# Performance work log

Measured on AMD Instinct MI355X. Metric: run time of the kernel, lower is better.

## Reference

```python
import jax, jax.numpy as jnp
import numpy as np

TAU = 0.1
BN_EPS = 1e-5


def setup_inputs() -> dict:
    key = jax.random.key(0)
    ks = jax.random.split(key, 10)
    bs, C, N, E, P = 2, 256, 4096, 2048, 32
    return {
        "vertex_feat": jax.random.normal(ks[0], (bs, C, N), dtype=jnp.float32),
        "incidence": jax.random.uniform(ks[1], (bs, N, E), dtype=jnp.float32),
        "inv_edge_degree": jax.random.uniform(ks[2], (bs, E, E), dtype=jnp.float32),
        "inv_vertex_degree": jax.random.uniform(ks[3], (bs, N, N), dtype=jnp.float32),
        "edge_scale": jax.random.uniform(ks[4], (bs, E, 1), dtype=jnp.float32),
        "proj_w": jax.random.normal(ks[5], (P, C), dtype=jnp.float32) * (1.0 / np.sqrt(C)),
        "bn_gamma": jax.random.uniform(ks[6], (P,), dtype=jnp.float32, minval=0.5, maxval=1.5),
        "bn_beta": jax.random.normal(ks[7], (P,), dtype=jnp.float32) * 0.1,
        "bn_mean": jax.random.normal(ks[8], (P,), dtype=jnp.float32) * 0.1,
        "bn_var": jax.random.uniform(ks[9], (P,), dtype=jnp.float32, minval=0.5, maxval=1.5),
    }


def reference(vertex_feat, incidence, inv_edge_degree, inv_vertex_degree, edge_scale,
              proj_w, bn_gamma, bn_beta, bn_mean, bn_var):
    # proj: 1x1 Conv1d [bs,C,N] -> [bs,P,N], then eval-mode BatchNorm1d over channel P
    K = jnp.einsum("pc,bcn->bpn", proj_w, vertex_feat)
    scale = (bn_gamma / jnp.sqrt(bn_var + BN_EPS))[None, :, None]
    K = (K - bn_mean[None, :, None]) * scale + bn_beta[None, :, None]
    K = jnp.transpose(K, (0, 2, 1))  # [bs, N, P]

    # edge prototypes: incidence^T @ K, normalized by inverse edge degree
    proto = jnp.einsum("bne,bnp->bep", incidence, K)          # [bs, E, P]
    proto = jnp.einsum("bef,bfp->bep", inv_edge_degree, proto)

    # squared L2 cost: ||proto_e||^2 + ||K_n||^2 - 2 <proto_e, K_n>
    K_sq = jnp.sum(K * K, axis=-1)[:, None, :]                 # [bs, 1, N]
    proto_sq = jnp.sum(proto * proto, axis=-1, keepdims=True)  # [bs, E, 1]
    inner = jnp.einsum("bep,bnp->ben", proto, K)               # [bs, E, N]
    cost = proto_sq + K_sq - 2.0 * inner

    weights = jax.nn.softmax(-cost / (TAU + 1e-8), axis=-1)    # [bs, E, N]

    # aggregate vertex features into edges
    edge_feat = jnp.einsum("ben,bcn->bec", weights, vertex_feat)   # [bs, E, C]
    edge_feat = jnp.einsum("bef,bfc->bec", inv_edge_degree, edge_feat)
    return jnp.transpose(edge_feat, (0, 2, 1))  # [bs, C, E]
```

## Files before the change

### kernel.cpp

```cpp
#include <hip/hip_runtime.h>
#include <math.h>

#define BS 2
#define C_DIM 256
#define N_DIM 4096
#define E_DIM 2048
#define P_DIM 32
#define NS1 32
#define FS2 8

typedef __attribute__((ext_vector_type(8))) short short8;
typedef __attribute__((ext_vector_type(4))) float f32x4;

__device__ __forceinline__ unsigned short f2bf(float f) {
  unsigned u = __float_as_uint(f);
  return (unsigned short)((u + 0x7FFFu + ((u >> 16) & 1u)) >> 16);
}

__global__ __launch_bounds__(256) void k_proj(
    const float* __restrict__ vf, const float* __restrict__ pw,
    const float* __restrict__ gamma, const float* __restrict__ beta,
    const float* __restrict__ mean, const float* __restrict__ var,
    float* __restrict__ Kf, float* __restrict__ Ksq) {
  __shared__ float w_s[P_DIM * C_DIM];
  __shared__ float part_s[4][64][P_DIM + 1];
  __shared__ float kt_s[64][P_DIM + 1];
  __shared__ float sc_s[P_DIM], sb_s[P_DIM], sm_s[P_DIM];

  const int tid = threadIdx.x;
  const int b = blockIdx.x >> 6;
  const int n0 = (blockIdx.x & 63) << 6;

  for (int i = tid; i < P_DIM * C_DIM; i += 256) w_s[i] = pw[i];
  if (tid < P_DIM) {
    sc_s[tid] = gamma[tid] / sqrtf(var[tid] + 1e-5f);
    sb_s[tid] = beta[tid];
    sm_s[tid] = mean[tid];
  }
  __syncthreads();

  const int nl = tid & 63, cs = tid >> 6;
  const float* vbase = vf + (size_t)b * C_DIM * N_DIM + n0 + nl;
  float acc[P_DIM];
#pragma unroll
  for (int p = 0; p < P_DIM; ++p) acc[p] = 0.f;
#pragma unroll 4
  for (int cc = 0; cc < 64; ++cc) {
    int c = cs * 64 + cc;
    float v = vbase[(size_t)c * N_DIM];
    const float* wc = &w_s[c];
#pragma unroll
    for (int p = 0; p < P_DIM; ++p) acc[p] = fmaf(wc[p * C_DIM], v, acc[p]);
  }
#pragma unroll
  for (int p = 0; p < P_DIM; ++p) part_s[cs][nl][p] = acc[p];
  __syncthreads();

  for (int i = tid; i < 64 * P_DIM; i += 256) {
    int n_l = i >> 5, p = i & 31;
    float s = ((part_s[0][n_l][p] + part_s[1][n_l][p]) + part_s[2][n_l][p]) +
              part_s[3][n_l][p];
    float k = (s - sm_s[p]) * sc_s[p] + sb_s[p];
    Kf[((size_t)(b * N_DIM + n0 + n_l)) * P_DIM + p] = k;
    kt_s[n_l][p] = k;
  }
  __syncthreads();
  if (tid < 64) {
    float q = 0.f;
#pragma unroll
    for (int p = 0; p < P_DIM; ++p) q = fmaf(kt_s[tid][p], kt_s[tid][p], q);
    Ksq[b * N_DIM + n0 + tid] = q;
  }
}

__global__ __launch_bounds__(256) void k_transpose(const float* __restrict__ vf,
                                                   float* __restrict__ VT) {
  __shared__ float t_s[64][65];
  const int tid = threadIdx.x;
  const int b = blockIdx.x >> 8;
  const int n0 = ((blockIdx.x >> 2) & 63) << 6;
  const int c0 = (blockIdx.x & 3) << 6;
  const float* src = vf + (size_t)b * C_DIM * N_DIM;
#pragma unroll
  for (int i = 0; i < 16; ++i) {
    int idx = tid + i * 256;
    int n_l = idx & 63, c_l = idx >> 6;
    t_s[c_l][n_l] = src[(size_t)(c0 + c_l) * N_DIM + n0 + n_l];
  }
  __syncthreads();
  float* dst = VT + (size_t)b * N_DIM * C_DIM;
#pragma unroll
  for (int i = 0; i < 16; ++i) {
    int idx = tid + i * 256;
    int c_l = idx & 63, n_l = idx >> 6;
    dst[(size_t)(n0 + n_l) * C_DIM + c0 + c_l] = t_s[c_l][n_l];
  }
}

__global__ __launch_bounds__(256) void k_proto1(const float* __restrict__ inc,
                                                const float* __restrict__ Kf,
                                                float* __restrict__ part) {
  __shared__ float k_s[64][P_DIM];
  const int tid = threadIdx.x;
  const int b = blockIdx.x >> 7;
  const int et = (blockIdx.x >> 5) & 3;
  const int ns = blockIdx.x & 31;
  const int e0 = et << 9;
  const int nbase = ns << 7;

  float acc0[P_DIM], acc1[P_DIM];
#pragma unroll
  for (int p = 0; p < P_DIM; ++p) { acc0[p] = 0.f; acc1[p] = 0.f; }

  for (int nt = 0; nt < 2; ++nt) {
    int n0 = nbase + nt * 64;
#pragma unroll
    for (int i = 0; i < 8; ++i) {
      int idx = tid + i * 256;
      ((float*)k_s)[idx] = Kf[((size_t)(b * N_DIM + n0)) * P_DIM + idx];
    }
    __syncthreads();
#pragma unroll 8
    for (int nn = 0; nn < 64; ++nn) {
      const float* irow = inc + ((size_t)(b * N_DIM + n0 + nn)) * E_DIM + e0;
      float va = irow[tid];
      float vb = irow[tid + 256];
      const float4* kv4 = (const float4*)k_s[nn];
#pragma unroll
      for (int q = 0; q < 8; ++q) {
        float4 kv = kv4[q];
        acc0[4 * q + 0] = fmaf(va, kv.x, acc0[4 * q + 0]);
        acc0[4 * q + 1] = fmaf(va, kv.y, acc0[4 * q + 1]);
        acc0[4 * q + 2] = fmaf(va, kv.z, acc0[4 * q + 2]);
        acc0[4 * q + 3] = fmaf(va, kv.w, acc0[4 * q + 3]);
        acc1[4 * q + 0] = fmaf(vb, kv.x, acc1[4 * q + 0]);
        acc1[4 * q + 1] = fmaf(vb, kv.y, acc1[4 * q + 1]);
        acc1[4 * q + 2] = fmaf(vb, kv.z, acc1[4 * q + 2]);
        acc1[4 * q + 3] = fmaf(vb, kv.w, acc1[4 * q + 3]);
      }
    }
    __syncthreads();
  }
  float* dst0 = part + (size_t)ns * (BS * E_DIM * P_DIM) +
                ((size_t)(b * E_DIM + e0 + tid)) * P_DIM;
  float* dst1 = dst0 + 256 * P_DIM;
#pragma unroll
  for (int q = 0; q < 8; ++q) {
    ((float4*)dst0)[q] = make_float4(acc0[4 * q + 0], acc0[4 * q + 1],
                                     acc0[4 * q + 2], acc0[4 * q + 3]);
    ((float4*)dst1)[q] = make_float4(acc1[4 * q + 0], acc1[4 * q + 1],
                                     acc1[4 * q + 2], acc1[4 * q + 3]);
  }
}

__global__ __launch_bounds__(256) void k_red32(const float* __restrict__ part,
                                               float* __restrict__ outp) {
  int g = blockIdx.x * 256 + threadIdx.x;
  float v = 0.f;
#pragma unroll
  for (int s = 0; s < NS1; ++s)
    v += part[(size_t)s * (BS * E_DIM * P_DIM) + g];
  outp[g] = v;
}

__global__ __launch_bounds__(256) void k_proto2(const float* __restrict__ ied,
                                                const float* __restrict__ proto1,
                                                float* __restrict__ part,
                                                short* __restrict__ ied_h) {
  __shared__ float inv_s[128][33];
  __shared__ float p1_s[32][P_DIM];
  const int tid = threadIdx.x;
  const int b = blockIdx.x >> 7;
  const int et = (blockIdx.x >> 3) & 15;
  const int fs = blockIdx.x & 7;
  const int e0 = et << 7;
  const int fbase = fs << 8;
  const int e_l = tid & 63, pg = tid >> 6;

  float acc0[8], acc1[8];
#pragma unroll
  for (int q = 0; q < 8; ++q) { acc0[q] = 0.f; acc1[q] = 0.f; }

  for (int ft = 0; ft < 8; ++ft) {
    int f0 = fbase + ft * 32;
    __syncthreads();
#pragma unroll
    for (int i = 0; i < 16; ++i) {
      int idx = tid + i * 256;
      int e_r = idx >> 5, f_l = idx & 31;
      size_t gidx = ((size_t)(b * E_DIM + e0 + e_r)) * E_DIM + f0 + f_l;
      float v = ied[gidx];
      inv_s[e_r][f_l] = v;
      ied_h[gidx] = (short)f2bf(v);
    }
#pragma unroll
    for (int i = 0; i < 4; ++i) {
      int idx = tid + i * 256;
      ((float*)p1_s)[idx] = proto1[((size_t)(b * E_DIM + f0)) * P_DIM + idx];
    }
    __syncthreads();
#pragma unroll
    for (int ff = 0; ff < 32; ++ff) {
      float a0 = inv_s[e_l][ff];
      float a1 = inv_s[e_l + 64][ff];
      const float4* pv4 = (const float4*)&p1_s[ff][pg * 8];
      float4 pv0 = pv4[0], pv1 = pv4[1];
      acc0[0] = fmaf(a0, pv0.x, acc0[0]);
      acc0[1] = fmaf(a0, pv0.y, acc0[1]);
      acc0[2] = fmaf(a0, pv0.z, acc0[2]);
      acc0[3] = fmaf(a0, pv0.w, acc0[3]);
      acc0[4] = fmaf(a0, pv1.x, acc0[4]);
      acc0[5] = fmaf(a0, pv1.y, acc0[5]);
      acc0[6] = fmaf(a0, pv1.z, acc0[6]);
      acc0[7] = fmaf(a0, pv1.w, acc0[7]);
      acc1[0] = fmaf(a1, pv0.x, acc1[0]);
      acc1[1] = fmaf(a1, pv0.y, acc1[1]);
      acc1[2] = fmaf(a1, pv0.z, acc1[2]);
      acc1[3] = fmaf(a1, pv0.w, acc1[3]);
      acc1[4] = fmaf(a1, pv1.x, acc1[4]);
      acc1[5] = fmaf(a1, pv1.y, acc1[5]);
      acc1[6] = fmaf(a1, pv1.z, acc1[6]);
      acc1[7] = fmaf(a1, pv1.w, acc1[7]);
    }
  }
  float* dst0 = part + (size_t)fs * (BS * E_DIM * P_DIM) +
                ((size_t)(b * E_DIM + e0 + e_l)) * P_DIM + pg * 8;
  float* dst1 = dst0 + 64 * P_DIM;
  ((float4*)dst0)[0] = make_float4(acc0[0], acc0[1], acc0[2], acc0[3]);
  ((float4*)dst0)[1] = make_float4(acc0[4], acc0[5], acc0[6], acc0[7]);
  ((float4*)dst1)[0] = make_float4(acc1[0], acc1[1], acc1[2], acc1[3]);
  ((float4*)dst1)[1] = make_float4(acc1[4], acc1[5], acc1[6], acc1[7]);
}

__global__ __launch_bounds__(256) void k_red8sq(const float* __restrict__ part,
                                                float* __restrict__ proto,
                                                float* __restrict__ psq) {
  int g = blockIdx.x * 256 + threadIdx.x;
  float v = 0.f;
#pragma unroll
  for (int s = 0; s < FS2; ++s)
    v += part[(size_t)s * (BS * E_DIM * P_DIM) + g];
  proto[g] = v;
  float q = v * v;
#pragma unroll
  for (int m = 1; m <= 16; m <<= 1) q += __shfl_xor(q, m, 64);
  if ((threadIdx.x & 31) == 0) psq[g >> 5] = q;
}

__global__ __launch_bounds__(256) void k_gmax(const float* __restrict__ Kf,
                                              const float* __restrict__ Ksq,
                                              const float* __restrict__ proto,
                                              float* __restrict__ chunkg) {
  __shared__ float a_s[P_DIM][64];
  __shared__ float b_s[P_DIM][64];
  __shared__ float q_s[64];
  const int tid = threadIdx.x;
  const int b = blockIdx.x >> 8;
  const int et = (blockIdx.x >> 3) & 31;
  const int ns = blockIdx.x & 7;
  const int e0 = et << 6;
  const int n0b = ns << 9;

  {
    int p = tid >> 6, e = tid & 63;
#pragma unroll
    for (int r = 0; r < 8; ++r)
      a_s[p + r * 4][e] =
          proto[((size_t)(b * E_DIM + e0 + e)) * P_DIM + p + r * 4];
  }
  const int te = tid >> 4, tn = tid & 15;
  float gm[4];
#pragma unroll
  for (int i = 0; i < 4; ++i) gm[i] = -INFINITY;

  for (int t = 0; t < 8; ++t) {
    const int n0 = n0b + t * 64;
    __syncthreads();
    {
      int p = tid >> 6, n = tid & 63;
#pragma unroll
      for (int r = 0; r < 8; ++r)
        b_s[p + r * 4][n] =
            Kf[((size_t)(b * N_DIM + n0 + n)) * P_DIM + p + r * 4];
      if (tid < 64) q_s[tid] = Ksq[b * N_DIM + n0 + tid];
    }
    __syncthreads();

    float acc[4][4];
#pragma unroll
    for (int i = 0; i < 4; ++i)
#pragma unroll
      for (int j = 0; j < 4; ++j) acc[i][j] = 0.f;

#pragma unroll
    for (int p = 0; p < P_DIM; ++p) {
      float4 av = *(const float4*)&a_s[p][te << 2];
      float4 bv = *(const float4*)&b_s[p][tn << 2];
      acc[0][0] = fmaf(av.x, bv.x, acc[0][0]);
      acc[0][1] = fmaf(av.x, bv.y, acc[0][1]);
      acc[0][2] = fmaf(av.x, bv.z, acc[0][2]);
      acc[0][3] = fmaf(av.x, bv.w, acc[0][3]);
      acc[1][0] = fmaf(av.y, bv.x, acc[1][0]);
      acc[1][1] = fmaf(av.y, bv.y, acc[1][1]);
      acc[1][2] = fmaf(av.y, bv.z, acc[1][2]);
      acc[1][3] = fmaf(av.y, bv.w, acc[1][3]);
      acc[2][0] = fmaf(av.z, bv.x, acc[2][0]);
      acc[2][1] = fmaf(av.z, bv.y, acc[2][1]);
      acc[2][2] = fmaf(av.z, bv.z, acc[2][2]);
      acc[2][3] = fmaf(av.z, bv.w, acc[2][3]);
      acc[3][0] = fmaf(av.w, bv.x, acc[3][0]);
      acc[3][1] = fmaf(av.w, bv.y, acc[3][1]);
      acc[3][2] = fmaf(av.w, bv.z, acc[3][2]);
      acc[3][3] = fmaf(av.w, bv.w, acc[3][3]);
    }
#pragma unroll
    for (int i = 0; i < 4; ++i)
#pragma unroll
      for (int j = 0; j < 4; ++j) {
        float g = fmaf(2.0f, acc[i][j], -q_s[(tn << 2) + j]);
        gm[i] = fmaxf(gm[i], g);
      }

    if (t & 1) {
#pragma unroll
      for (int i = 0; i < 4; ++i) {
        float v = gm[i];
        v = fmaxf(v, __shfl_xor(v, 1, 64));
        v = fmaxf(v, __shfl_xor(v, 2, 64));
        v = fmaxf(v, __shfl_xor(v, 4, 64));
        v = fmaxf(v, __shfl_xor(v, 8, 64));
        if (tn == 0)
          chunkg[((size_t)(b * E_DIM + e0 + (te << 2) + i)) * 32 + (ns << 2) +
                 (t >> 1)] = v;
        gm[i] = -INFINITY;
      }
    }
  }
}

__device__ __forceinline__ float edge_logit(const float* __restrict__ Kb,
                                            const float* __restrict__ Qb,
                                            const float* pr, float psqv,
                                            int n) {
  const float4* kp = (const float4*)(Kb + (size_t)n * P_DIM);
  float i0 = 0.f, i1 = 0.f, i2 = 0.f, i3 = 0.f;
#pragma unroll
  for (int q = 0; q < 8; ++q) {
    float4 kv = kp[q];
    i0 = fmaf(pr[4 * q + 0], kv.x, i0);
    i1 = fmaf(pr[4 * q + 1], kv.y, i1);
    i2 = fmaf(pr[4 * q + 2], kv.z, i2);
    i3 = fmaf(pr[4 * q + 3], kv.w, i3);
  }
  float inner = (i0 + i1) + (i2 + i3);
  float cost = fmaf(-2.0f, inner, psqv + Qb[n]);
  const float tau_eps = 0.1f + 1e-8f;
  return (-cost) / tau_eps;
}

__global__ __launch_bounds__(256) void k_sparse(
    const float* __restrict__ Kf, const float* __restrict__ Ksq,
    const float* __restrict__ proto, const float* __restrict__ psq,
    const float* __restrict__ VT, const float* __restrict__ chunkg,
    float* __restrict__ EF0) {
  const int tid = threadIdx.x;
  const int lane = tid & 63;
  const int eg = blockIdx.x * 4 + (tid >> 6);
  const int b = eg >> 11;
  const float* Kb = Kf + (size_t)b * N_DIM * P_DIM;
  const float* Qb = Ksq + (size_t)b * N_DIM;

  float cg = (lane < 32) ? chunkg[(size_t)eg * 32 + lane] : -INFINITY;
  float gmax = cg;
#pragma unroll
  for (int m = 1; m <= 32; m <<= 1) gmax = fmaxf(gmax, __shfl_xor(gmax, m, 64));
  unsigned long long live = __ballot(cg > gmax - 20.0f);

  float pr[P_DIM];
  const float* pe = proto + (size_t)eg * P_DIM;
#pragma unroll
  for (int p = 0; p < P_DIM; ++p) pr[p] = pe[p];
  const float psqv = psq[eg];

  float L = -INFINITY;
  unsigned long long m0 = live;
  while (m0) {
    int c = __ffsll(m0) - 1;
    m0 &= m0 - 1;
    int n = (c << 7) + lane;
    L = fmaxf(L, edge_logit(Kb, Qb, pr, psqv, n));
    L = fmaxf(L, edge_logit(Kb, Qb, pr, psqv, n + 64));
  }
#pragma unroll
  for (int m = 1; m <= 32; m <<= 1) L = fmaxf(L, __shfl_xor(L, m, 64));

  float4 acc = make_float4(0.f, 0.f, 0.f, 0.f);
  float sw = 0.f;
  const float* Vb = VT + (size_t)b * N_DIM * C_DIM;
  m0 = live;
  while (m0) {
    int c = __ffsll(m0) - 1;
    m0 &= m0 - 1;
#pragma unroll
    for (int h = 0; h < 2; ++h) {
      int n = (c << 7) + (h << 6) + lane;
      float l = edge_logit(Kb, Qb, pr, psqv, n);
      float d = l - L;
      float wgt = (d > -25.0f) ? expf(d) : 0.f;
      sw += wgt;
      unsigned long long hits = __ballot(wgt > 0.f);
      while (hits) {
        int src = __ffsll(hits) - 1;
        hits &= hits - 1;
        float wv = __shfl(wgt, src, 64);
        int nv = (c << 7) + (h << 6) + src;
        const float4 vrow =
            *(const float4*)(Vb + (size_t)nv * C_DIM + (lane << 2));
        acc.x = fmaf(wv, vrow.x, acc.x);
        acc.y = fmaf(wv, vrow.y, acc.y);
        acc.z = fmaf(wv, vrow.z, acc.z);
        acc.w = fmaf(wv, vrow.w, acc.w);
      }
    }
  }
#pragma unroll
  for (int m = 1; m <= 32; m <<= 1) sw += __shfl_xor(sw, m, 64);

  float* dst = EF0 + (size_t)eg * C_DIM + (lane << 2);
  *(float4*)dst =
      make_float4(acc.x / sw, acc.y / sw, acc.z / sw, acc.w / sw);
}

__global__ __launch_bounds__(256) void k_ef0t(const float* __restrict__ EF0,
                                              short* __restrict__ EF0t) {
  __shared__ short sh[64][72];
  const int tid = threadIdx.x;
  const int b = blockIdx.x >> 7;
  const int ft = (blockIdx.x >> 2) & 31;
  const int ct = blockIdx.x & 3;
  const int f0 = ft << 6, c0 = ct << 6;
#pragma unroll
  for (int i = 0; i < 4; ++i) {
    int idx = tid + i * 256;
    int f_l = idx >> 4, cc = idx & 15;
    float4 v =
        *(const float4*)&EF0[((size_t)(b * E_DIM + f0 + f_l)) * C_DIM + c0 +
                             cc * 4];
    sh[cc * 4 + 0][f_l] = (short)f2bf(v.x);
    sh[cc * 4 + 1][f_l] = (short)f2bf(v.y);
    sh[cc * 4 + 2][f_l] = (short)f2bf(v.z);
    sh[cc * 4 + 3][f_l] = (short)f2bf(v.w);
  }
  __syncthreads();
#pragma unroll
  for (int i = 0; i < 2; ++i) {
    int idx = tid + i * 256;
    int c_l = idx >> 3, ch = idx & 7;
    short8 v = *(const short8*)&sh[c_l][ch * 8];
    *(short8*)&EF0t[((size_t)(b * C_DIM + c0 + c_l)) * E_DIM + f0 + ch * 8] = v;
  }
}

__device__ __forceinline__ short8 lds_frag(const short* s, int row, int k) {
  int off = (((row << 6) + k) << 1) ^ ((row & 7) << 4);
  return *(const short8*)((const char*)s + off);
}
__device__ __forceinline__ void lds_put(short* s, int row, int k, short8 v) {
  int off = (((row << 6) + k) << 1) ^ ((row & 7) << 4);
  *(short8*)((char*)s + off) = v;
}

__global__ __launch_bounds__(256) void k_final_mfma(
    const short* __restrict__ Ah, const short* __restrict__ Bh,
    float* __restrict__ out) {
  __shared__ short As[2][64 * 64];
  __shared__ short Bs[2][64 * 64];
  __shared__ float Cs[64][68];

  const int tid = threadIdx.x;
  const int lane = tid & 63;
  const int w = tid >> 6;
  const int ct = blockIdx.x & 3;
  const int et = (blockIdx.x >> 2) & 31;
  const int b = blockIdx.x >> 7;
  const int e0 = et << 6, c0 = ct << 6;

  const int we = (w >> 1) << 5;
  const int wc = (w & 1) << 5;
  const int row = tid >> 2, ch = tid & 3;

  const short* gA = Ah + ((size_t)(b * E_DIM + e0 + row)) * E_DIM;
  const short* gB = Bh + ((size_t)(b * C_DIM + c0 + row)) * E_DIM;

  f32x4 z = {0.f, 0.f, 0.f, 0.f};
  f32x4 acc00 = z, acc01 = z, acc10 = z, acc11 = z;

  {
    const short8* pa = (const short8*)(gA + ch * 16);
    const short8* pb = (const short8*)(gB + ch * 16);
    short8 a0 = pa[0], a1 = pa[1];
    short8 b0 = pb[0], b1 = pb[1];
    lds_put(As[0], row, ch * 16, a0);
    lds_put(As[0], row, ch * 16 + 8, a1);
    lds_put(Bs[0], row, ch * 16, b0);
    lds_put(Bs[0], row, ch * 16 + 8, b1);
  }
  __syncthreads();

  for (int kt = 0; kt < 32; ++kt) {
    const int cur = kt & 1;
    short8 na0, na1, nb0, nb1;
    if (kt < 31) {
      const int f1 = (kt + 1) << 6;
      const short8* pa = (const short8*)(gA + f1 + ch * 16);
      const short8* pb = (const short8*)(gB + f1 + ch * 16);
      na0 = pa[0]; na1 = pa[1]; nb0 = pb[0]; nb1 = pb[1];
    }
#pragma unroll
    for (int s = 0; s < 2; ++s) {
      const int kb = (s << 5) + ((lane >> 4) << 3);
      short8 fa0 = lds_frag(As[cur], we + (lane & 15), kb);
      short8 fa1 = lds_frag(As[cur], we + 16 + (lane & 15), kb);
      short8 fb0 = lds_frag(Bs[cur], wc + (lane & 15), kb);
      short8 fb1 = lds_frag(Bs[cur], wc + 16 + (lane & 15), kb);
      acc00 = __builtin_amdgcn_mfma_f32_16x16x32_bf16(fa0, fb0, acc00, 0, 0, 0);
      acc01 = __builtin_amdgcn_mfma_f32_16x16x32_bf16(fa0, fb1, acc01, 0, 0, 0);
      acc10 = __builtin_amdgcn_mfma_f32_16x16x32_bf16(fa1, fb0, acc10, 0, 0, 0);
      acc11 = __builtin_amdgcn_mfma_f32_16x16x32_bf16(fa1, fb1, acc11, 0, 0, 0);
    }
    if (kt < 31) {
      lds_put(As[cur ^ 1], row, ch * 16, na0);
      lds_put(As[cur ^ 1], row, ch * 16 + 8, na1);
      lds_put(Bs[cur ^ 1], row, ch * 16, nb0);
      lds_put(Bs[cur ^ 1], row, ch * 16 + 8, nb1);
    }
    __syncthreads();
  }

  const int fr = lane & 15, fq = lane >> 4;
#pragma unroll
  for (int r = 0; r < 4; ++r) {
    Cs[wc + fr][we + fq * 4 + r] = acc00[r];
    Cs[wc + 16 + fr][we + fq * 4 + r] = acc01[r];
    Cs[wc + fr][we + 16 + fq * 4 + r] = acc10[r];
    Cs[wc + 16 + fr][we + 16 + fq * 4 + r] = acc11[r];
  }
  __syncthreads();
  {
    const int c_l = tid >> 2, cch = tid & 3;
    float* dst = out + ((size_t)(b * C_DIM + c0 + c_l)) * E_DIM + e0;
#pragma unroll
    for (int r = 0; r < 4; ++r) {
      float4 v = *(const float4*)&Cs[c_l][cch * 16 + r * 4];
      *(float4*)&dst[cch * 16 + r * 4] = v;
    }
  }
}

extern "C" void kernel_launch(void* const* d_in, const int* in_sizes, int n_in,
                              void* d_out, int out_size, void* d_ws,
                              size_t ws_size, hipStream_t stream) {
  (void)in_sizes; (void)n_in; (void)out_size; (void)ws_size;
  const float* vf  = (const float*)d_in[0];
  const float* inc = (const float*)d_in[1];
  const float* ied = (const float*)d_in[2];
  const float* pw  = (const float*)d_in[5];
  const float* gm  = (const float*)d_in[6];
  const float* bt  = (const float*)d_in[7];
  const float* mn  = (const float*)d_in[8];
  const float* vr  = (const float*)d_in[9];
  float* out = (float*)d_out;

  float* ws = (float*)d_ws;
  float* VT      = ws;
  float* Kf      = VT + 2097152;
  float* Ksq     = Kf + 262144;
  float* proto1  = Ksq + 8192;
  float* proto   = proto1 + 131072;
  float* psq     = proto + 131072;
  float* P1p     = psq + 4096;
  float* P2p     = P1p + 4194304;
  float* EF0     = P2p + 1048576;
  float* chunkg  = EF0 + 1048576;
  short* ied_h   = (short*)(chunkg + 131072);
  short* EF0t    = (short*)(chunkg + 131072 + 4194304);

  k_proj<<<dim3(128), dim3(256), 0, stream>>>(vf, pw, gm, bt, mn, vr, Kf, Ksq);
  k_transpose<<<dim3(512), dim3(256), 0, stream>>>(vf, VT);
  k_proto1<<<dim3(256), dim3(256), 0, stream>>>(inc, Kf, P1p);
  k_red32<<<dim3(512), dim3(256), 0, stream>>>(P1p, proto1);
  k_proto2<<<dim3(256), dim3(256), 0, stream>>>(ied, proto1, P2p, ied_h);
  k_red8sq<<<dim3(512), dim3(256), 0, stream>>>(P2p, proto, psq);
  k_gmax<<<dim3(512), dim3(256), 0, stream>>>(Kf, Ksq, proto, chunkg);
  k_sparse<<<dim3(1024), dim3(256), 0, stream>>>(Kf, Ksq, proto, psq, VT,
                                                 chunkg, EF0);
  k_ef0t<<<dim3(256), dim3(256), 0, stream>>>(EF0, EF0t);
  k_final_mfma<<<dim3(256), dim3(256), 0, stream>>>(ied_h, EF0t, out);
}
```

Baseline: 158.6 us.

## Restructure k_gmax to one 128-vertex chunk per block with 4x8 register tiles

The chunk-max kernel now handles a single 64-edge by 128-vertex tile per block instead of looping over eight 64-vertex tiles. The grid grows from 512 to 2048 blocks and per-block barriers drop to one. Each thread computes a 4x8 output tile and writes the chunk max directly. Global loads are now coalesced along the P dimension. The aim is more parallelism and less per-block serial looping and synchronisation, at the cost of reloading the proto tile once per chunk and more registers per thread.

```diff
diff --git a/kernel.cpp b/kernel.cpp
--- a/kernel.cpp
+++ b/kernel.cpp
@@ -252,89 +252,80 @@
                                               const float* __restrict__ proto,
                                               float* __restrict__ chunkg) {
   __shared__ float a_s[P_DIM][64];
-  __shared__ float b_s[P_DIM][64];
-  __shared__ float q_s[64];
-  const int tid = threadIdx.x;
-  const int b = blockIdx.x >> 8;
-  const int et = (blockIdx.x >> 3) & 31;
-  const int ns = blockIdx.x & 7;
+  __shared__ float b_s[P_DIM][128];
+  __shared__ float q_s[128];
+  const int tid = threadIdx.x;
+  const int b = blockIdx.x >> 10;
+  const int et = (blockIdx.x >> 5) & 31;
+  const int ch = blockIdx.x & 31;
   const int e0 = et << 6;
-  const int n0b = ns << 9;
-
-  {
-    int p = tid >> 6, e = tid & 63;
-#pragma unroll
-    for (int r = 0; r < 8; ++r)
-      a_s[p + r * 4][e] =
-          proto[((size_t)(b * E_DIM + e0 + e)) * P_DIM + p + r * 4];
-  }
-  const int te = tid >> 4, tn = tid & 15;
-  float gm[4];
-#pragma unroll
-  for (int i = 0; i < 4; ++i) gm[i] = -INFINITY;
-
-  for (int t = 0; t < 8; ++t) {
-    const int n0 = n0b + t * 64;
-    __syncthreads();
-    {
-      int p = tid >> 6, n = tid & 63;
-#pragma unroll
-      for (int r = 0; r < 8; ++r)
-        b_s[p + r * 4][n] =
-            Kf[((size_t)(b * N_DIM + n0 + n)) * P_DIM + p + r * 4];
-      if (tid < 64) q_s[tid] = Ksq[b * N_DIM + n0 + tid];
-    }
-    __syncthreads();
-
-    float acc[4][4];
-#pragma unroll
-    for (int i = 0; i < 4; ++i)
-#pragma unroll
-      for (int j = 0; j < 4; ++j) acc[i][j] = 0.f;
-
-#pragma unroll
-    for (int p = 0; p < P_DIM; ++p) {
-      float4 av = *(const float4*)&a_s[p][te << 2];
-      float4 bv = *(const float4*)&b_s[p][tn << 2];
-      acc[0][0] = fmaf(av.x, bv.x, acc[0][0]);
-      acc[0][1] = fmaf(av.x, bv.y, acc[0][1]);
-      acc[0][2] = fmaf(av.x, bv.z, acc[0][2]);
-      acc[0][3] = fmaf(av.x, bv.w, acc[0][3]);
-      acc[1][0] = fmaf(av.y, bv.x, acc[1][0]);
-      acc[1][1] = fmaf(av.y, bv.y, acc[1][1]);
-      acc[1][2] = fmaf(av.y, bv.z, acc[1][2]);
-      acc[1][3] = fmaf(av.y, bv.w, acc[1][3]);
-      acc[2][0] = fmaf(av.z, bv.x, acc[2][0]);
-      acc[2][1] = fmaf(av.z, bv.y, acc[2][1]);
-      acc[2][2] = fmaf(av.z, bv.z, acc[2][2]);
-      acc[2][3] = fmaf(av.z, bv.w, acc[2][3]);
-      acc[3][0] = fmaf(av.w, bv.x, acc[3][0]);
-      acc[3][1] = fmaf(av.w, bv.y, acc[3][1]);
-      acc[3][2] = fmaf(av.w, bv.z, acc[3][2]);
-      acc[3][3] = fmaf(av.w, bv.w, acc[3][3]);
-    }
-#pragma unroll
-    for (int i = 0; i < 4; ++i)
-#pragma unroll
-      for (int j = 0; j < 4; ++j) {
-        float g = fmaf(2.0f, acc[i][j], -q_s[(tn << 2) + j]);
-        gm[i] = fmaxf(gm[i], g);
-      }
-
-    if (t & 1) {
-#pragma unroll
-      for (int i = 0; i < 4; ++i) {
-        float v = gm[i];
-        v = fmaxf(v, __shfl_xor(v, 1, 64));
-        v = fmaxf(v, __shfl_xor(v, 2, 64));
-        v = fmaxf(v, __shfl_xor(v, 4, 64));
-        v = fmaxf(v, __shfl_xor(v, 8, 64));
-        if (tn == 0)
-          chunkg[((size_t)(b * E_DIM + e0 + (te << 2) + i)) * 32 + (ns << 2) +
-                 (t >> 1)] = v;
-        gm[i] = -INFINITY;
-      }
-    }
+  const int n0 = ch << 7;
+
+#pragma unroll
+  for (int i = 0; i < 8; ++i) {
+    int idx = tid + i * 256;
+    int e = idx >> 5, p = idx & 31;
+    a_s[p][e] = proto[((size_t)(b * E_DIM + e0 + e)) * P_DIM + p];
+  }
+#pragma unroll
+  for (int i = 0; i < 16; ++i) {
+    int idx = tid + i * 256;
+    int n = idx >> 5, p = idx & 31;
+    b_s[p][n] = Kf[((size_t)(b * N_DIM + n0 + n)) * P_DIM + p];
+  }
+  if (tid < 128) q_s[tid] = Ksq[b * N_DIM + n0 + tid];
+  __syncthreads();
+
+  const int te = tid >> 4, j = tid & 15;
+  f32x4 z = {0.f, 0.f, 0.f, 0.f};
+  f32x4 a0a = z, a0b = z, a1a = z, a1b = z;
+  f32x4 a2a = z, a2b = z, a3a = z, a3b = z;
+
+#pragma unroll
+  for (int p = 0; p < P_DIM; ++p) {
+    float4 av = *(const float4*)&a_s[p][te << 2];
+    float4 b0 = *(const float4*)&b_s[p][j << 3];
+    float4 b1 = *(const float4*)&b_s[p][(j << 3) + 4];
+    a0a.x = fmaf(av.x, b0.x, a0a.x); a0a.y = fmaf(av.x, b0.y, a0a.y);
+    a0a.z = fmaf(av.x, b0.z, a0a.z); a0a.w = fmaf(av.x, b0.w, a0a.w);
+    a0b.x = fmaf(av.x, b1.x, a0b.x); a0b.y = fmaf(av.x, b1.y, a0b.y);
+    a0b.z = fmaf(av.x, b1.z, a0b.z); a0b.w = fmaf(av.x, b1.w, a0b.w);
+    a1a.x = fmaf(av.y, b0.x, a1a.x); a1a.y = fmaf(av.y, b0.y, a1a.y);
+    a1a.z = fmaf(av.y, b0.z, a1a.z); a1a.w = fmaf(av.y, b0.w, a1a.w);
+    a1b.x = fmaf(av.y, b1.x, a1b.x); a1b.y = fmaf(av.y, b1.y, a1b.y);
+    a1b.z = fmaf(av.y, b1.z, a1b.z); a1b.w = fmaf(av.y, b1.w, a1b.w);
+    a2a.x = fmaf(av.z, b0.x, a2a.x); a2a.y = fmaf(av.z, b0.y, a2a.y);
+    a2a.z = fmaf(av.z, b0.z, a2a.z); a2a.w = fmaf(av.z, b0.w, a2a.w);
+    a2b.x = fmaf(av.z, b1.x, a2b.x); a2b.y = fmaf(av.z, b1.y, a2b.y);
+    a2b.z = fmaf(av.z, b1.z, a2b.z); a2b.w = fmaf(av.z, b1.w, a2b.w);
+    a3a.x = fmaf(av.w, b0.x, a3a.x); a3a.y = fmaf(av.w, b0.y, a3a.y);
+    a3a.z = fmaf(av.w, b0.z, a3a.z); a3a.w = fmaf(av.w, b0.w, a3a.w);
+    a3b.x = fmaf(av.w, b1.x, a3b.x); a3b.y = fmaf(av.w, b1.y, a3b.y);
+    a3b.z = fmaf(av.w, b1.z, a3b.z); a3b.w = fmaf(av.w, b1.w, a3b.w);
+  }
+
+  const int qb = j << 3;
+  float q0 = q_s[qb + 0], q1 = q_s[qb + 1], q2 = q_s[qb + 2], q3 = q_s[qb + 3];
+  float q4 = q_s[qb + 4], q5 = q_s[qb + 5], q6 = q_s[qb + 6], q7 = q_s[qb + 7];
+
+#pragma unroll
+  for (int r = 0; r < 4; ++r) {
+    f32x4 pa = (r == 0) ? a0a : (r == 1) ? a1a : (r == 2) ? a2a : a3a;
+    f32x4 pb = (r == 0) ? a0b : (r == 1) ? a1b : (r == 2) ? a2b : a3b;
+    float m = fmaf(2.0f, pa.x, -q0);
+    m = fmaxf(m, fmaf(2.0f, pa.y, -q1));
+    m = fmaxf(m, fmaf(2.0f, pa.z, -q2));
+    m = fmaxf(m, fmaf(2.0f, pa.w, -q3));
+    m = fmaxf(m, fmaf(2.0f, pb.x, -q4));
+    m = fmaxf(m, fmaf(2.0f, pb.y, -q5));
+    m = fmaxf(m, fmaf(2.0f, pb.z, -q6));
+    m = fmaxf(m, fmaf(2.0f, pb.w, -q7));
+    m = fmaxf(m, __shfl_xor(m, 1, 64));
+    m = fmaxf(m, __shfl_xor(m, 2, 64));
+    m = fmaxf(m, __shfl_xor(m, 4, 64));
+    m = fmaxf(m, __shfl_xor(m, 8, 64));
+    if (j == 0)
+      chunkg[((size_t)(b * E_DIM + e0 + (te << 2) + r)) * 32 + ch] = m;
   }
 }
 
@@ -591,7 +582,7 @@
   k_red32<<<dim3(512), dim3(256), 0, stream>>>(P1p, proto1);
   k_proto2<<<dim3(256), dim3(256), 0, stream>>>(ied, proto1, P2p, ied_h);
   k_red8sq<<<dim3(512), dim3(256), 0, stream>>>(P2p, proto, psq);
-  k_gmax<<<dim3(512), dim3(256), 0, stream>>>(Kf, Ksq, proto, chunkg);
+  k_gmax<<<dim3(2048), dim3(256), 0, stream>>>(Kf, Ksq, proto, chunkg);
   k_sparse<<<dim3(1024), dim3(256), 0, stream>>>(Kf, Ksq, proto, psq, VT,
                                                  chunkg, EF0);
   k_ef0t<<<dim3(256), dim3(256), 0, stream>>>(EF0, EF0t);
```

Measured after the change: 205.9 us. +29.8%, slower.
